# Optimization experiments

Measured on AMD Instinct MI355X. Metric: run time of the kernel, lower is better.

The kernel has to match this reference:

```python
import jax, jax.numpy as jnp
import numpy as np

N_NODES = 50000
N_EDGES = 800000
IN_DIM = 128
HID_DIM = 64
OUT_DIM = 40
N_REL = 8


def setup_inputs() -> dict:
    key = jax.random.key(0)
    ks = jax.random.split(key, 12)
    x = jax.random.normal(ks[0], (N_NODES, IN_DIM), dtype=jnp.float32)
    edge_index = jax.random.randint(ks[1], (2, N_EDGES), 0, N_NODES, dtype=jnp.int64)
    edge_type = jax.random.randint(ks[2], (N_EDGES,), 0, N_REL, dtype=jnp.int64)
    s = 0.05
    W1 = jax.random.normal(ks[3], (N_REL, IN_DIM, HID_DIM), dtype=jnp.float32) * s
    root1 = jax.random.normal(ks[4], (IN_DIM, HID_DIM), dtype=jnp.float32) * s
    b1 = jnp.zeros((HID_DIM,), dtype=jnp.float32)
    W2 = jax.random.normal(ks[5], (N_REL, HID_DIM, HID_DIM), dtype=jnp.float32) * s
    root2 = jax.random.normal(ks[6], (HID_DIM, HID_DIM), dtype=jnp.float32) * s
    b2 = jnp.zeros((HID_DIM,), dtype=jnp.float32)
    Wl = jax.random.normal(ks[7], (HID_DIM, OUT_DIM), dtype=jnp.float32) * s
    bl = jnp.zeros((OUT_DIM,), dtype=jnp.float32)
    return {"x": x, "edge_index": edge_index, "edge_type": edge_type,
            "W1": W1, "root1": root1, "b1": b1,
            "W2": W2, "root2": root2, "b2": b2,
            "Wl": Wl, "bl": bl}


def _rgcn_conv(x, W, Wroot, b, src, dst, edge_type):
    # PyG RGCNConv (no bases/blocks, aggr='mean'):
    #   out[i] = sum_r mean_{(j->i) of rel r} (x[j] @ W[r]) + x[i] @ Wroot + b
    N = x.shape[0]
    R = W.shape[0]
    h = jnp.einsum('ni,rio->rno', x, W)        # [R, N, out]
    msgs = h[edge_type, src]                   # [E, out] edge gather
    seg = edge_type * N + dst                  # per (relation, dst) segment
    sums = jax.ops.segment_sum(msgs, seg, num_segments=R * N)
    cnt = jax.ops.segment_sum(jnp.ones((msgs.shape[0],), x.dtype), seg,
                              num_segments=R * N)
    mean = sums / jnp.maximum(cnt, 1.0)[:, None]
    agg = mean.reshape(R, N, -1).sum(axis=0)   # sum over relations
    return agg + x @ Wroot + b


def reference(x, edge_index, edge_type, W1, root1, b1, W2, root2, b2, Wl, bl):
    src, dst = edge_index[0], edge_index[1]
    h = jax.nn.relu(_rgcn_conv(x, W1, root1, b1, src, dst, edge_type))
    # dropout is identity in eval mode
    h = jax.nn.relu(_rgcn_conv(h, W2, root2, b2, src, dst, edge_type))
    logits = h @ Wl + bl
    return jax.nn.log_softmax(logits, axis=1)
```

## Files before the change

### kernel.cpp

```cpp
#include <hip/hip_runtime.h>
#include <hip/hip_bf16.h>
#include <cmath>

#define IN_DIM 128
#define HID 64
#define OUT_DIM 40
#define NREL 8
#define NCOLS 576
#define CAP 64
#define CSTR 16

typedef __attribute__((ext_vector_type(8))) short short8;
typedef __attribute__((ext_vector_type(4))) short short4v;
typedef __attribute__((ext_vector_type(4))) float floatx4;
typedef __attribute__((ext_vector_type(2))) float f32x2;

static __device__ __forceinline__ short f2bf(float f) {
  __hip_bfloat16 h = __float2bfloat16(f);
  return __builtin_bit_cast(short, h);
}
static __device__ __forceinline__ float bflo(unsigned int u) {
  return __int_as_float(u << 16);
}
static __device__ __forceinline__ float bfhi(unsigned int u) {
  return __int_as_float(u & 0xffff0000u);
}
static __device__ __forceinline__ unsigned int packbf(float x, float y) {
  unsigned int lo = (unsigned short)f2bf(x);
  unsigned int hi = (unsigned short)f2bf(y);
  return lo | (hi << 16);
}

__global__ void pack_bt(const float* __restrict__ W1, const float* __restrict__ root1,
                        short* __restrict__ Bt1,
                        const float* __restrict__ W2, const float* __restrict__ root2,
                        short* __restrict__ Bt2) {
  const int PB1 = (NCOLS * IN_DIM + 255) / 256;
  int b = blockIdx.x;
  if (b < PB1) {
    int i = b * 256 + threadIdx.x;
    if (i >= NCOLS * IN_DIM) return;
    int c = i / IN_DIM, k = i % IN_DIM;
    float v = (c < NREL * HID)
      ? W1[((size_t)(c >> 6) * IN_DIM + k) * HID + (c & 63)]
      : root1[(size_t)k * HID + (c - NREL * HID)];
    Bt1[i] = f2bf(v);
  } else {
    int i = (b - PB1) * 256 + threadIdx.x;
    if (i >= NCOLS * HID) return;
    int c = i / HID, k = i % HID;
    float v = (c < NREL * HID)
      ? W2[((size_t)(c >> 6) * HID + k) * HID + (c & 63)]
      : root2[(size_t)k * HID + (c - NREL * HID)];
    Bt2[i] = f2bf(v);
  }
}

template<int K, int AMODE>
__device__ __forceinline__ void gemm_dev(
    short* As, short* Bs,
    const void* __restrict__ Aptr, const short* __restrict__ Bt,
    const float* __restrict__ bias, short* __restrict__ H,
    unsigned short* __restrict__ AGG, int M, int row0)
{
  constexpr int AST = K + 8;
  int tid = threadIdx.x;
  int wv = tid >> 6, lane = tid & 63;
  int lm = lane & 15, quad = lane >> 4;

  if (AMODE == 0) {
    const float* A = (const float*)Aptr;
    constexpr int CH = K / 4;
    for (int i = tid; i < 64 * CH; i += 256) {
      int r = i / CH, kq = i % CH;
      int gr = row0 + r; if (gr >= M) gr = M - 1;
      float4 v = *(const float4*)(A + (unsigned)(gr * K + kq * 4));
      short4v s;
      s.x = f2bf(v.x); s.y = f2bf(v.y); s.z = f2bf(v.z); s.w = f2bf(v.w);
      *(short4v*)(As + r * AST + kq * 4) = s;
    }
  } else {
    const short* A = (const short*)Aptr;
    constexpr int CH = K / 8;
    for (int i = tid; i < 64 * CH; i += 256) {
      int r = i / CH, ko = i % CH;
      int gr = row0 + r; if (gr >= M) gr = M - 1;
      short8 v = *(const short8*)(A + (unsigned)(gr * K + ko * 8));
      #pragma unroll
      for (int j = 0; j < 8; ++j)
        if ((unsigned short)v[j] & 0x8000u) v[j] = 0;
      *(short8*)(As + r * AST + ko * 8) = v;
    }
  }

  const short* ap = As + (16 * wv + lm) * AST + quad * 8;

  for (int cy = 0; cy < 9; ++cy) {
    constexpr int CB = K / 8;
    for (int i = tid; i < 64 * CB; i += 256) {
      int n = i / CB, ko = i % CB;
      short8 v = *(const short8*)(Bt + (unsigned)((cy * 64 + n) * K + ko * 8));
      *(short8*)(Bs + n * AST + ko * 8) = v;
    }
    __syncthreads();

    floatx4 acc[4] = {{0,0,0,0},{0,0,0,0},{0,0,0,0},{0,0,0,0}};
    #pragma unroll
    for (int ks = 0; ks < K / 32; ++ks) {
      short8 a = *(const short8*)(ap + ks * 32);
      #pragma unroll
      for (int nb = 0; nb < 4; ++nb) {
        short8 b = *(const short8*)(Bs + (nb * 16 + lm) * AST + ks * 32 + quad * 8);
        acc[nb] = __builtin_amdgcn_mfma_f32_16x16x32_bf16(a, b, acc[nb], 0, 0, 0);
      }
    }
    __syncthreads();

    int mbase = row0 + 16 * wv + quad * 4;
    if (cy < 8) {
      #pragma unroll
      for (int nb = 0; nb < 4; ++nb) {
        int col = cy * 64 + nb * 16 + lm;
        #pragma unroll
        for (int r = 0; r < 4; ++r) {
          int mg = mbase + r;
          if (mg < M) H[(unsigned)mg * (NREL * HID) + col] = f2bf(acc[nb][r]);
        }
      }
    } else {
      #pragma unroll
      for (int nb = 0; nb < 4; ++nb) {
        int col = nb * 16 + lm;
        float bv = bias[col];
        #pragma unroll
        for (int r = 0; r < 4; ++r) {
          int mg = mbase + r;
          if (mg < M)
            AGG[(unsigned)mg * HID + col] = (unsigned short)f2bf(acc[nb][r] + bv);
        }
      }
    }
  }
}

__global__ __launch_bounds__(256, 4) void gemm1_scatter(
    const float* __restrict__ A, const short* __restrict__ Bt,
    const float* __restrict__ bias, short* __restrict__ H,
    unsigned short* __restrict__ AGG, int M, int GB,
    const int* __restrict__ src, const int* __restrict__ dst,
    const int* __restrict__ et,
    int* __restrict__ cursor, int* __restrict__ ev, int E)
{
  constexpr int AST = IN_DIM + 8;
  __shared__ short As[64 * AST];
  __shared__ short Bs[64 * AST];
  if ((int)blockIdx.x < GB) {
    gemm_dev<IN_DIM, 0>(As, Bs, A, Bt, bias, H, AGG, M, blockIdx.x * 64);
  } else {
    int e = (blockIdx.x - GB) * 256 + threadIdx.x;
    if (e >= E) return;
    int d = dst[e];
    int pos = atomicAdd(&cursor[d * CSTR], 1);
    if (pos < CAP)
      __builtin_nontemporal_store((src[e] << 3) | et[e], &ev[d * CAP + pos]);
  }
}

__global__ __launch_bounds__(256, 4) void gemm2_mfma(
    const unsigned short* __restrict__ A, const short* __restrict__ Bt,
    const float* __restrict__ bias, short* __restrict__ H,
    unsigned short* __restrict__ AGG, int M)
{
  constexpr int AST = HID + 8;
  __shared__ short As[64 * AST];
  __shared__ short Bs[64 * AST];
  gemm_dev<HID, 1>(As, Bs, A, Bt, bias, H, AGG, M, blockIdx.x * 64);
}

__global__ __launch_bounds__(256) void finalize_ev(
    const int* __restrict__ cursor, int* __restrict__ ev, int N)
{
  int d = blockIdx.x * 4 + (threadIdx.x >> 6);
  if (d >= N) return;
  int lane = threadIdx.x & 63;
  int cnt = cursor[d * CSTR]; if (cnt > CAP) cnt = CAP;
  int e = (lane < cnt) ? ev[d * CAP + lane] : 0;
  int t = e & 7;
  int code = 64;
  #pragma unroll
  for (int r = 0; r < 8; ++r) {
    unsigned long long m = __ballot(lane < cnt && t == r);
    int c = __popcll(m);
    if (lane < cnt && t == r) code = c - 1;
  }
  ev[d * CAP + lane] = (lane < cnt) ? ((e << 7) | code) : 64;
}

static __device__ __forceinline__ void agg_half(
    const uint2* __restrict__ Hu2, const int* __restrict__ evrow,
    int npass, int qloc, int sub, const float* __restrict__ lut,
    float& a0, float& a1, float& a2, float& a3)
{
  f32x2 A01 = {a0, a1}, A23 = {a2, a3};
  for (int P = 0; P < npass; ++P) {
    const int4* pp = (const int4*)(evrow + P * 16 + qloc * 8);
    int4 v0 = pp[0], v1 = pp[1];
    int vv[8] = {v0.x, v0.y, v0.z, v0.w, v1.x, v1.y, v1.z, v1.w};
    uint2 hv[8];
    float ww[8];
    #pragma unroll
    for (int i = 0; i < 8; ++i) {
      hv[i] = Hu2[(unsigned)(vv[i] >> 7) * 16u + (unsigned)sub];
      ww[i] = lut[vv[i] & 127];
    }
    #pragma unroll
    for (int i = 0; i < 8; ++i) {
      f32x2 w2 = {ww[i], ww[i]};
      f32x2 h01 = {bflo(hv[i].x), bfhi(hv[i].x)};
      f32x2 h23 = {bflo(hv[i].y), bfhi(hv[i].y)};
      A01 += h01 * w2;
      A23 += h23 * w2;
    }
  }
  a0 = A01.x; a1 = A01.y; a2 = A23.x; a3 = A23.y;
  a0 += __shfl_xor(a0, 16, 64);
  a1 += __shfl_xor(a1, 16, 64);
  a2 += __shfl_xor(a2, 16, 64);
  a3 += __shfl_xor(a3, 16, 64);
}

__global__ __launch_bounds__(256) void csr_agg(
    const short* __restrict__ H, const int* __restrict__ cursor,
    const int* __restrict__ ev, unsigned short* __restrict__ AGG, int N)
{
  __shared__ float lut[128];
  int tid = threadIdx.x;
  if (tid < 128) lut[tid] = (tid < 64) ? 1.0f / (float)(tid + 1) : 0.f;
  __syncthreads();

  int wv = tid >> 6, lane = tid & 63;
  int h = lane >> 5, lhl = lane & 31, qloc = lhl >> 4, sub = lhl & 15;
  int d = blockIdx.x * 8 + wv * 2 + h;
  if (d >= N) return;

  int cnt = cursor[d * CSTR]; if (cnt > CAP) cnt = CAP;
  float a0 = 0.f, a1 = 0.f, a2 = 0.f, a3 = 0.f;
  uint2* aggrow = (uint2*)(AGG + (size_t)d * HID);
  if (qloc == 0) {
    uint2 iv = aggrow[sub];
    a0 = bflo(iv.x); a1 = bfhi(iv.x); a2 = bflo(iv.y); a3 = bfhi(iv.y);
  }
  int npass = (cnt + 15) >> 4;
  if (npass > 0)
    agg_half((const uint2*)H, ev + d * CAP, npass, qloc, sub, lut, a0, a1, a2, a3);
  if (qloc == 0) {
    uint2 ov;
    ov.x = packbf(a0, a1);
    ov.y = packbf(a2, a3);
    aggrow[sub] = ov;
  }
}

__global__ __launch_bounds__(256) void csr_agg_final(
    const short* __restrict__ H, const int* __restrict__ cursor,
    const int* __restrict__ ev, const unsigned short* __restrict__ AGG,
    const float* __restrict__ Wl, const float* __restrict__ bl,
    float* __restrict__ out, int N)
{
  __shared__ float sWl[HID * OUT_DIM];
  __shared__ float sbl[OUT_DIM];
  __shared__ float sh[8][HID];
  __shared__ float lut[128];
  int tid = threadIdx.x;
  int wv = tid >> 6, lane = tid & 63;
  int h = lane >> 5, lhl = lane & 31, qloc = lhl >> 4, sub = lhl & 15;
  int d = blockIdx.x * 8 + wv * 2 + h;
  int dc = d < N ? d : N - 1;

  int cnt = cursor[dc * CSTR]; if (cnt > CAP) cnt = CAP;
  uint2 iv = ((const uint2*)(AGG + (size_t)dc * HID))[sub];

  for (int i = tid; i < HID * OUT_DIM; i += 256) sWl[i] = Wl[i];
  if (tid < OUT_DIM) sbl[tid] = bl[tid];
  if (tid < 128) lut[tid] = (tid < 64) ? 1.0f / (float)(tid + 1) : 0.f;
  __syncthreads();

  float a0 = 0.f, a1 = 0.f, a2 = 0.f, a3 = 0.f;
  if (qloc == 0) {
    a0 = bflo(iv.x); a1 = bfhi(iv.x); a2 = bflo(iv.y); a3 = bfhi(iv.y);
  }
  int npass = (cnt + 15) >> 4;
  if (npass > 0)
    agg_half((const uint2*)H, ev + dc * CAP, npass, qloc, sub, lut, a0, a1, a2, a3);
  if (qloc == 0) {
    float4 v;
    v.x = fmaxf(a0, 0.f); v.y = fmaxf(a1, 0.f);
    v.z = fmaxf(a2, 0.f); v.w = fmaxf(a3, 0.f);
    *(float4*)(&sh[wv * 2 + h][4 * sub]) = v;
  }
  __syncthreads();

  #pragma unroll
  for (int ii = 0; ii < 2; ++ii) {
    int dd = blockIdx.x * 8 + wv * 2 + ii;
    const float* row = sh[wv * 2 + ii];
    float logit = -__builtin_inff();
    if (lane < OUT_DIM) {
      float t = sbl[lane];
      #pragma unroll 8
      for (int k = 0; k < HID; ++k) t += row[k] * sWl[k * OUT_DIM + lane];
      logit = t;
    }
    float m = logit;
    #pragma unroll
    for (int o = 32; o > 0; o >>= 1) m = fmaxf(m, __shfl_xor(m, o, 64));
    float ex = (lane < OUT_DIM) ? expf(logit - m) : 0.f;
    float s = ex;
    #pragma unroll
    for (int o = 32; o > 0; o >>= 1) s += __shfl_xor(s, o, 64);
    if (dd < N && lane < OUT_DIM)
      out[(size_t)dd * OUT_DIM + lane] = logit - m - logf(s);
  }
}

extern "C" void kernel_launch(void* const* d_in, const int* in_sizes, int n_in,
                              void* d_out, int out_size, void* d_ws, size_t ws_size,
                              hipStream_t stream) {
  const float* x     = (const float*)d_in[0];
  const int*   eidx  = (const int*)d_in[1];
  const int*   etype = (const int*)d_in[2];
  const float* W1    = (const float*)d_in[3];
  const float* root1 = (const float*)d_in[4];
  const float* b1    = (const float*)d_in[5];
  const float* W2    = (const float*)d_in[6];
  const float* root2 = (const float*)d_in[7];
  const float* b2    = (const float*)d_in[8];
  const float* Wl    = (const float*)d_in[9];
  const float* bl    = (const float*)d_in[10];

  int N = in_sizes[0] / IN_DIM;
  int E = in_sizes[2];
  const int* srcp = eidx;
  const int* dstp = eidx + E;

  char* ws = (char*)d_ws;
  size_t off = 0;
  auto alloc = [&](size_t bytes) -> char* {
    char* p = ws + off;
    off += (bytes + 255) & ~(size_t)255;
    return p;
  };
  short* Bt1    = (short*)alloc((size_t)NCOLS * IN_DIM * 2);
  short* Bt2    = (short*)alloc((size_t)NCOLS * HID * 2);
  int*   cursor = (int*)alloc((size_t)N * CSTR * 4);
  int*   ev     = (int*)alloc((size_t)N * CAP * 4);
  short* H1     = (short*)alloc((size_t)N * NREL * HID * 2);
  short* H2     = (short*)alloc((size_t)N * NREL * HID * 2);
  unsigned short* AGG1 = (unsigned short*)alloc((size_t)N * HID * 2);
  unsigned short* AGG2 = (unsigned short*)alloc((size_t)N * HID * 2);

  hipMemsetAsync(cursor, 0, (size_t)N * CSTR * 4, stream);

  const int PB1 = (NCOLS * IN_DIM + 255) / 256;
  const int PB2 = (NCOLS * HID + 255) / 256;
  pack_bt<<<PB1 + PB2, 256, 0, stream>>>(W1, root1, Bt1, W2, root2, Bt2);

  int GB = (N + 63) / 64;
  int SB = (E + 255) / 256;
  gemm1_scatter<<<GB + SB, 256, 0, stream>>>(x, Bt1, b1, H1, AGG1, N, GB,
                                             srcp, dstp, etype, cursor, ev, E);

  finalize_ev<<<(N + 3) / 4, 256, 0, stream>>>(cursor, ev, N);

  csr_agg<<<(N + 7) / 8, 256, 0, stream>>>(H1, cursor, ev, AGG1, N);

  gemm2_mfma<<<GB, 256, 0, stream>>>(AGG1, Bt2, b2, H2, AGG2, N);

  csr_agg_final<<<(N + 7) / 8, 256, 0, stream>>>(H2, cursor, ev, AGG2,
                                                 Wl, bl, (float*)d_out, N);
}
```

Before: 229.7 us.

## Double-buffer B tiles via direct LDS loads, fuse finalize and memset

The GEMM B-tile staging now uses async global_load_lds into a double-buffered, XOR-swizzled LDS buffer, so the next tile loads while the current one is multiplied. This removes the padded copy and one barrier per cycle. The finalize_ev kernel is removed: per-relation mean weights are computed inline in the aggregation kernels with ballots and shuffles. The cursor memset is folded into pack_bt, and the edge scatter processes four edges per thread with batched loads. Together these drop two launches, at the cost of more LDS and redundant weight computation in both aggregation passes.

```diff
diff --git a/kernel.cpp b/kernel.cpp
--- a/kernel.cpp
+++ b/kernel.cpp
@@ -1,6 +1,7 @@
 #include <hip/hip_runtime.h>
 #include <hip/hip_bf16.h>
 #include <cmath>
+
 
 #define IN_DIM 128
 #define HID 64
@@ -31,11 +32,19 @@
   return lo | (hi << 16);
 }
 
+static __device__ __forceinline__ void gload_lds16(const void* g, void* l) {
+  __builtin_amdgcn_global_load_lds(
+      (const __attribute__((address_space(1))) unsigned int*)g,
+      (__attribute__((address_space(3))) unsigned int*)l, 16, 0, 0);
+}
+
 __global__ void pack_bt(const float* __restrict__ W1, const float* __restrict__ root1,
                         short* __restrict__ Bt1,
                         const float* __restrict__ W2, const float* __restrict__ root2,
-                        short* __restrict__ Bt2) {
+                        short* __restrict__ Bt2,
+                        int* __restrict__ cursor, int nzero4) {
   const int PB1 = (NCOLS * IN_DIM + 255) / 256;
+  const int PB2 = (NCOLS * HID + 255) / 256;
   int b = blockIdx.x;
   if (b < PB1) {
     int i = b * 256 + threadIdx.x;
@@ -45,7 +54,7 @@
       ? W1[((size_t)(c >> 6) * IN_DIM + k) * HID + (c & 63)]
       : root1[(size_t)k * HID + (c - NREL * HID)];
     Bt1[i] = f2bf(v);
-  } else {
+  } else if (b < PB1 + PB2) {
     int i = (b - PB1) * 256 + threadIdx.x;
     if (i >= NCOLS * HID) return;
     int c = i / HID, k = i % HID;
@@ -53,6 +62,26 @@
       ? W2[((size_t)(c >> 6) * HID + k) * HID + (c & 63)]
       : root2[(size_t)k * HID + (c - NREL * HID)];
     Bt2[i] = f2bf(v);
+  } else {
+    int i = (b - PB1 - PB2) * 256 + threadIdx.x;
+    if (i < nzero4) {
+      int4 z; z.x = 0; z.y = 0; z.z = 0; z.w = 0;
+      ((int4*)cursor)[i] = z;
+    }
+  }
+}
+
+template<int K>
+static __device__ __forceinline__ void stage_b_tile(
+    const short* __restrict__ tb, short* bufp, int wv, int lane) {
+  constexpr int GR = K / 8;
+  constexpr int CALLS = GR / 4;
+  #pragma unroll
+  for (int j = 0; j < CALLS; ++j) {
+    int c = wv * CALLS + j;
+    int s = c * 64 + lane;
+    int row = s / GR, g = s % GR;
+    gload_lds16(tb + (row * GR + (g ^ (row & 7))) * 8, bufp + c * 512);
   }
 }
 
@@ -63,10 +92,12 @@
     const float* __restrict__ bias, short* __restrict__ H,
     unsigned short* __restrict__ AGG, int M, int row0)
 {
-  constexpr int AST = K + 8;
+  constexpr int ASTA = K + 8;
   int tid = threadIdx.x;
   int wv = tid >> 6, lane = tid & 63;
   int lm = lane & 15, quad = lane >> 4;
+
+  stage_b_tile<K>(Bt, Bs, wv, lane);
 
   if (AMODE == 0) {
     const float* A = (const float*)Aptr;
@@ -77,7 +108,7 @@
       float4 v = *(const float4*)(A + (unsigned)(gr * K + kq * 4));
       short4v s;
       s.x = f2bf(v.x); s.y = f2bf(v.y); s.z = f2bf(v.z); s.w = f2bf(v.w);
-      *(short4v*)(As + r * AST + kq * 4) = s;
+      *(short4v*)(As + r * ASTA + kq * 4) = s;
     }
   } else {
     const short* A = (const short*)Aptr;
@@ -89,20 +120,19 @@
       #pragma unroll
       for (int j = 0; j < 8; ++j)
         if ((unsigned short)v[j] & 0x8000u) v[j] = 0;
-      *(short8*)(As + r * AST + ko * 8) = v;
-    }
-  }
-
-  const short* ap = As + (16 * wv + lm) * AST + quad * 8;
+      *(short8*)(As + r * ASTA + ko * 8) = v;
+    }
+  }
+
+  __syncthreads();
+
+  const short* ap = As + (16 * wv + lm) * ASTA + quad * 8;
+  const int swz = lm & 7;
 
   for (int cy = 0; cy < 9; ++cy) {
-    constexpr int CB = K / 8;
-    for (int i = tid; i < 64 * CB; i += 256) {
-      int n = i / CB, ko = i % CB;
-      short8 v = *(const short8*)(Bt + (unsigned)((cy * 64 + n) * K + ko * 8));
-      *(short8*)(Bs + n * AST + ko * 8) = v;
-    }
-    __syncthreads();
+    const short* buf = Bs + (cy & 1) * (64 * K);
+    if (cy < 8)
+      stage_b_tile<K>(Bt + (cy + 1) * (64 * K), Bs + ((cy + 1) & 1) * (64 * K), wv, lane);
 
     floatx4 acc[4] = {{0,0,0,0},{0,0,0,0},{0,0,0,0},{0,0,0,0}};
     #pragma unroll
@@ -110,11 +140,11 @@
       short8 a = *(const short8*)(ap + ks * 32);
       #pragma unroll
       for (int nb = 0; nb < 4; ++nb) {
-        short8 b = *(const short8*)(Bs + (nb * 16 + lm) * AST + ks * 32 + quad * 8);
+        short8 b = *(const short8*)(buf + (nb * 16 + lm) * K +
+                                    (((ks * 4 + quad) ^ swz) * 8));
         acc[nb] = __builtin_amdgcn_mfma_f32_16x16x32_bf16(a, b, acc[nb], 0, 0, 0);
       }
     }
-    __syncthreads();
 
     int mbase = row0 + 16 * wv + quad * 4;
     if (cy < 8) {
@@ -140,6 +170,7 @@
         }
       }
     }
+    if (cy < 8) __syncthreads();
   }
 }
 
@@ -151,18 +182,27 @@
     const int* __restrict__ et,
     int* __restrict__ cursor, int* __restrict__ ev, int E)
 {
-  constexpr int AST = IN_DIM + 8;
-  __shared__ short As[64 * AST];
-  __shared__ short Bs[64 * AST];
+  __shared__ short As[64 * (IN_DIM + 8)];
+  __shared__ short Bs[2 * 64 * IN_DIM];
   if ((int)blockIdx.x < GB) {
     gemm_dev<IN_DIM, 0>(As, Bs, A, Bt, bias, H, AGG, M, blockIdx.x * 64);
   } else {
-    int e = (blockIdx.x - GB) * 256 + threadIdx.x;
-    if (e >= E) return;
-    int d = dst[e];
-    int pos = atomicAdd(&cursor[d * CSTR], 1);
-    if (pos < CAP)
-      __builtin_nontemporal_store((src[e] << 3) | et[e], &ev[d * CAP + pos]);
+    int base = (blockIdx.x - GB) * 1024 + threadIdx.x;
+    int dd[4], ss[4], tt[4];
+    #pragma unroll
+    for (int u = 0; u < 4; ++u) {
+      int e = base + u * 256;
+      int ec = (e < E) ? e : 0;
+      dd[u] = dst[ec]; ss[u] = src[ec]; tt[u] = et[ec];
+    }
+    #pragma unroll
+    for (int u = 0; u < 4; ++u) {
+      int e = base + u * 256;
+      if (e < E) {
+        int pos = atomicAdd(&cursor[dd[u] * CSTR], 1);
+        if (pos < CAP) ev[dd[u] * CAP + pos] = (ss[u] << 3) | tt[u];
+      }
+    }
   }
 }
 
@@ -171,47 +211,32 @@
     const float* __restrict__ bias, short* __restrict__ H,
     unsigned short* __restrict__ AGG, int M)
 {
-  constexpr int AST = HID + 8;
-  __shared__ short As[64 * AST];
-  __shared__ short Bs[64 * AST];
+  __shared__ short As[64 * (HID + 8)];
+  __shared__ short Bs[2 * 64 * HID];
   gemm_dev<HID, 1>(As, Bs, A, Bt, bias, H, AGG, M, blockIdx.x * 64);
 }
 
-__global__ __launch_bounds__(256) void finalize_ev(
-    const int* __restrict__ cursor, int* __restrict__ ev, int N)
-{
-  int d = blockIdx.x * 4 + (threadIdx.x >> 6);
-  if (d >= N) return;
-  int lane = threadIdx.x & 63;
-  int cnt = cursor[d * CSTR]; if (cnt > CAP) cnt = CAP;
-  int e = (lane < cnt) ? ev[d * CAP + lane] : 0;
-  int t = e & 7;
-  int code = 64;
-  #pragma unroll
-  for (int r = 0; r < 8; ++r) {
-    unsigned long long m = __ballot(lane < cnt && t == r);
-    int c = __popcll(m);
-    if (lane < cnt && t == r) code = c - 1;
-  }
-  ev[d * CAP + lane] = (lane < cnt) ? ((e << 7) | code) : 64;
-}
-
-static __device__ __forceinline__ void agg_half(
+static __device__ __forceinline__ void agg_half2(
     const uint2* __restrict__ Hu2, const int* __restrict__ evrow,
-    int npass, int qloc, int sub, const float* __restrict__ lut,
+    int cnt, int qloc, int sub, float wreg, int h,
     float& a0, float& a1, float& a2, float& a3)
 {
+  int npass = (cnt + 15) >> 4;
   f32x2 A01 = {a0, a1}, A23 = {a2, a3};
   for (int P = 0; P < npass; ++P) {
     const int4* pp = (const int4*)(evrow + P * 16 + qloc * 8);
     int4 v0 = pp[0], v1 = pp[1];
     int vv[8] = {v0.x, v0.y, v0.z, v0.w, v1.x, v1.y, v1.z, v1.w};
+    int sb = P * 16 + qloc * 8;
     uint2 hv[8];
     float ww[8];
     #pragma unroll
     for (int i = 0; i < 8; ++i) {
-      hv[i] = Hu2[(unsigned)(vv[i] >> 7) * 16u + (unsigned)sub];
-      ww[i] = lut[vv[i] & 127];
+      bool ok = (sb + i) < cnt;
+      int v = ok ? vv[i] : 0;
+      hv[i] = Hu2[(unsigned)v * 16u + (unsigned)sub];
+      float w = __shfl(wreg, h * 32 + (v & 7), 64);
+      ww[i] = ok ? w : 0.f;
     }
     #pragma unroll
     for (int i = 0; i < 8; ++i) {
@@ -229,31 +254,47 @@
   a3 += __shfl_xor(a3, 16, 64);
 }
 
+static __device__ __forceinline__ float rel_weight(
+    const int* __restrict__ evr, int cnt, int lhl, int h)
+{
+  int e0 = evr[lhl], e1 = evr[lhl + 32];
+  bool v0 = lhl < cnt, v1 = (lhl + 32) < cnt;
+  int r0 = e0 & 7, r1 = e1 & 7;
+  unsigned long long hm = 0xffffffffull << (h * 32);
+  int myrel = lhl & 7;
+  int c = 0;
+  #pragma unroll
+  for (int r = 0; r < 8; ++r) {
+    unsigned long long m0 = __ballot(v0 && (r0 == r));
+    unsigned long long m1 = __ballot(v1 && (r1 == r));
+    int cr = __popcll(m0 & hm) + __popcll(m1 & hm);
+    if (myrel == r) c = cr;
+  }
+  return (c > 0) ? (1.0f / (float)c) : 0.0f;
+}
+
 __global__ __launch_bounds__(256) void csr_agg(
     const short* __restrict__ H, const int* __restrict__ cursor,
     const int* __restrict__ ev, unsigned short* __restrict__ AGG, int N)
 {
-  __shared__ float lut[128];
   int tid = threadIdx.x;
-  if (tid < 128) lut[tid] = (tid < 64) ? 1.0f / (float)(tid + 1) : 0.f;
-  __syncthreads();
-
   int wv = tid >> 6, lane = tid & 63;
   int h = lane >> 5, lhl = lane & 31, qloc = lhl >> 4, sub = lhl & 15;
   int d = blockIdx.x * 8 + wv * 2 + h;
-  if (d >= N) return;
-
-  int cnt = cursor[d * CSTR]; if (cnt > CAP) cnt = CAP;
+  int dc = d < N ? d : N - 1;
+
+  int cnt = cursor[dc * CSTR]; if (cnt > CAP) cnt = CAP;
+  const int* evr = ev + dc * CAP;
+  float wreg = rel_weight(evr, cnt, lhl, h);
+
   float a0 = 0.f, a1 = 0.f, a2 = 0.f, a3 = 0.f;
-  uint2* aggrow = (uint2*)(AGG + (size_t)d * HID);
+  uint2* aggrow = (uint2*)(AGG + (size_t)dc * HID);
   if (qloc == 0) {
     uint2 iv = aggrow[sub];
     a0 = bflo(iv.x); a1 = bfhi(iv.x); a2 = bflo(iv.y); a3 = bfhi(iv.y);
   }
-  int npass = (cnt + 15) >> 4;
-  if (npass > 0)
-    agg_half((const uint2*)H, ev + d * CAP, npass, qloc, sub, lut, a0, a1, a2, a3);
-  if (qloc == 0) {
+  agg_half2((const uint2*)H, evr, cnt, qloc, sub, wreg, h, a0, a1, a2, a3);
+  if (d < N && qloc == 0) {
     uint2 ov;
     ov.x = packbf(a0, a1);
     ov.y = packbf(a2, a3);
@@ -270,7 +311,6 @@
   __shared__ float sWl[HID * OUT_DIM];
   __shared__ float sbl[OUT_DIM];
   __shared__ float sh[8][HID];
-  __shared__ float lut[128];
   int tid = threadIdx.x;
   int wv = tid >> 6, lane = tid & 63;
   int h = lane >> 5, lhl = lane & 31, qloc = lhl >> 4, sub = lhl & 15;
@@ -279,19 +319,18 @@
 
   int cnt = cursor[dc * CSTR]; if (cnt > CAP) cnt = CAP;
   uint2 iv = ((const uint2*)(AGG + (size_t)dc * HID))[sub];
+  const int* evr = ev + dc * CAP;
+  float wreg = rel_weight(evr, cnt, lhl, h);
 
   for (int i = tid; i < HID * OUT_DIM; i += 256) sWl[i] = Wl[i];
   if (tid < OUT_DIM) sbl[tid] = bl[tid];
-  if (tid < 128) lut[tid] = (tid < 64) ? 1.0f / (float)(tid + 1) : 0.f;
   __syncthreads();
 
   float a0 = 0.f, a1 = 0.f, a2 = 0.f, a3 = 0.f;
   if (qloc == 0) {
     a0 = bflo(iv.x); a1 = bfhi(iv.x); a2 = bflo(iv.y); a3 = bfhi(iv.y);
   }
-  int npass = (cnt + 15) >> 4;
-  if (npass > 0)
-    agg_half((const uint2*)H, ev + dc * CAP, npass, qloc, sub, lut, a0, a1, a2, a3);
+  agg_half2((const uint2*)H, evr, cnt, qloc, sub, wreg, h, a0, a1, a2, a3);
   if (qloc == 0) {
     float4 v;
     v.x = fmaxf(a0, 0.f); v.y = fmaxf(a1, 0.f);
@@ -359,19 +398,18 @@
   unsigned short* AGG1 = (unsigned short*)alloc((size_t)N * HID * 2);
   unsigned short* AGG2 = (unsigned short*)alloc((size_t)N * HID * 2);
 
-  hipMemsetAsync(cursor, 0, (size_t)N * CSTR * 4, stream);
-
   const int PB1 = (NCOLS * IN_DIM + 255) / 256;
   const int PB2 = (NCOLS * HID + 255) / 256;
-  pack_bt<<<PB1 + PB2, 256, 0, stream>>>(W1, root1, Bt1, W2, root2, Bt2);
+  int nzero4 = (N * CSTR) / 4;
+  int ZB = (nzero4 + 255) / 256;
+  pack_bt<<<PB1 + PB2 + ZB, 256, 0, stream>>>(W1, root1, Bt1, W2, root2, Bt2,
+                                              cursor, nzero4);
 
   int GB = (N + 63) / 64;
-  int SB = (E + 255) / 256;
+  int SB = (E + 1023) / 1024;
   gemm1_scatter<<<GB + SB, 256, 0, stream>>>(x, Bt1, b1, H1, AGG1, N, GB,
                                              srcp, dstp, etype, cursor, ev, E);
 
-  finalize_ev<<<(N + 3) / 4, 256, 0, stream>>>(cursor, ev, N);
-
   csr_agg<<<(N + 7) / 8, 256, 0, stream>>>(H1, cursor, ev, AGG1, N);
 
   gemm2_mfma<<<GB, 256, 0, stream>>>(AGG1, Bt2, b2, H2, AGG2, N);
```

Result: slower. 249.0 us (+8.4%).
